# Optimization experiments

Hardware: AMD Instinct MI355X
Metric: run time of the kernel (lower is better)

## Reference

```python
import jax, jax.numpy as jnp
import numpy as np

MAX_ANGLES = 6
SCALES = 2
BN_EPS = 1e-5


def _gauss(k):
    # Gaussian filter init used by WaveletTransform1D (kernel_size k, sigma=k/4)
    xs = np.arange(k, dtype=np.float32) - k // 2
    w = np.exp(-xs ** 2 / (2.0 * (k / 4.0) ** 2)).astype(np.float32)
    return jnp.asarray((w / w.sum()).reshape(1, 1, k))


def setup_inputs():
    key = jax.random.key(0)
    ks = jax.random.split(key, 8)
    B, C, H, W = 8, 64, 128, 128
    return {
        "x": jax.random.normal(ks[0], (B, C, H, W), jnp.float32),
        "lin1_w": jax.random.normal(ks[1], (32, C * 16), jnp.float32) * 0.02,
        "lin1_b": jnp.zeros((32,), jnp.float32),
        "lin2_w": jax.random.normal(ks[2], (MAX_ANGLES, 32), jnp.float32) * 0.02,
        "lin2_b": jnp.zeros((MAX_ANGLES,), jnp.float32),
        "wf0": _gauss(3),
        "wf1": _gauss(5),
        "fuse_w": jax.random.normal(ks[3], (C, C * SCALES), jnp.float32) * 0.05,
        "fuse_b": jax.random.normal(ks[4], (C,), jnp.float32) * 0.05,
        "bn_gamma": jnp.ones((C,), jnp.float32),
        "bn_beta": jnp.zeros((C,), jnp.float32),
        "bn_mean": jnp.zeros((C,), jnp.float32),
        "bn_var": jnp.ones((C,), jnp.float32),
    }


def _grid_sample(img, grid):
    # torch F.grid_sample, bilinear, align_corners=True, padding_mode='zeros'
    N, C, H, W = img.shape
    ix = (grid[..., 0] + 1.0) * 0.5 * (W - 1)  # (N,Hg,Wg)
    iy = (grid[..., 1] + 1.0) * 0.5 * (H - 1)
    x0 = jnp.floor(ix)
    y0 = jnp.floor(iy)
    wx = ix - x0
    wy = iy - y0

    def gather(xi, yi):
        valid = (xi >= 0) & (xi <= W - 1) & (yi >= 0) & (yi <= H - 1)
        xc = jnp.clip(xi, 0, W - 1).astype(jnp.int32)
        yc = jnp.clip(yi, 0, H - 1).astype(jnp.int32)
        v = jax.vmap(lambda im, yy, xx: im[:, yy, xx])(img, yc, xc)  # (N,C,Hg,Wg)
        return v * valid[:, None, :, :].astype(img.dtype)

    v00 = gather(x0, y0)
    v01 = gather(x0 + 1, y0)
    v10 = gather(x0, y0 + 1)
    v11 = gather(x0 + 1, y0 + 1)
    return (v00 * ((1 - wx) * (1 - wy))[:, None]
            + v01 * (wx * (1 - wy))[:, None]
            + v10 * ((1 - wx) * wy)[:, None]
            + v11 * (wx * wy)[:, None])


def _interp1d(x, Lout):
    # F.interpolate mode='linear', align_corners=False, over last axis
    Lin = x.shape[-1]
    real = jnp.clip((jnp.arange(Lout, dtype=jnp.float32) + 0.5) * (Lin / Lout) - 0.5, 0.0, Lin - 1.0)
    i0 = jnp.floor(real).astype(jnp.int32)
    i1 = jnp.minimum(i0 + 1, Lin - 1)
    w = real - i0
    return x[..., i0] * (1.0 - w) + x[..., i1] * w


def _interp_last_ac(x, Lout):
    # linear interp over last axis, align_corners=True
    Lin = x.shape[-1]
    if Lin == Lout:
        return x
    pos = jnp.arange(Lout, dtype=jnp.float32) * ((Lin - 1) / (Lout - 1))
    i0 = jnp.floor(pos).astype(jnp.int32)
    i1 = jnp.minimum(i0 + 1, Lin - 1)
    w = pos - i0
    return x[..., i0] * (1.0 - w) + x[..., i1] * w


def _avgpool1(x):
    L = x.shape[-1]
    return x[..., : (L // 2) * 2].reshape(x.shape[:-1] + (L // 2, 2)).mean(-1)


def _conv1(sig, w):
    # sig (N,1,L), w (1,1,k), 'same' padding cross-correlation (matches torch Conv1d)
    k = w.shape[-1]
    return jax.lax.conv_general_dilated(sig, w, (1,), [(k // 2, k // 2)],
                                        dimension_numbers=("NCH", "OIH", "NCH"))


def reference(x, lin1_w, lin1_b, lin2_w, lin2_b, wf0, wf1, fuse_w, fuse_b,
              bn_gamma, bn_beta, bn_mean, bn_var):
    B, C, H, W = x.shape
    K = MAX_ANGLES
    # --- AnglePredictor: adaptive avg pool 4x4 (H,W divisible by 4) + MLP ---
    pooled = x.reshape(B, C, 4, H // 4, 4, W // 4).mean(axis=(3, 5))  # (B,C,4,4)
    feat = pooled.reshape(B, C * 16)
    h = jax.nn.relu(feat @ lin1_w.T + lin1_b)
    off = (h @ lin2_w.T + lin2_b) * 30.0
    base = jnp.linspace(0.0, 180.0, K)
    angles = jnp.sort(jnp.clip(base[None, :] + off, 0.0, 180.0), axis=1)  # (B,K)
    # --- RadonTransform: per-angle rotation grid + grid_sample + sum over W ---
    xs = jnp.linspace(-1.0, 1.0, W)
    ys = jnp.linspace(-1.0, 1.0, H)
    yc, xc = jnp.meshgrid(ys, xs, indexing="ij")
    th = angles * (jnp.pi / 180.0)
    co = jnp.cos(th)[:, :, None, None]
    si = jnp.sin(th)[:, :, None, None]
    gx = xc[None, None] * co + yc[None, None] * si
    gy = -xc[None, None] * si + yc[None, None] * co
    grid = jnp.stack([gx, gy], axis=-1).reshape(B * K, H, W, 2)
    xexp = jnp.broadcast_to(x[:, None], (B, K, C, H, W)).reshape(B * K, C, H, W)
    rotated = _grid_sample(xexp, grid)          # (B*K,C,H,W)
    sig = rotated.sum(axis=3)                   # (B*K,C,H) == sinogram permuted
    # --- WaveletTransform1D (2 scales, L=H=128 > 4) ---
    N = B * K
    c0 = _conv1(sig.reshape(N * C, 1, H), wf0).reshape(N, C, H)
    cur = _avgpool1(sig)                        # (N,C,H//2)
    L2 = H // 2
    f1 = _conv1(cur.reshape(N * C, 1, L2), wf1)
    u1 = _interp1d(_avgpool1(f1), L2).reshape(N, C, L2)
    c1 = _interp1d(u1, H)                       # resized to target length H
    coeffs = jnp.stack([c0, c1], axis=2)        # (N,C,SCALES,H)
    wav = coeffs.reshape(B, K, C, SCALES, H).transpose(0, 2, 4, 3, 1)  # (B,C,H,S,K)
    combined = wav.reshape(B, C * SCALES, H, K)  # matches torch .view on contiguous
    # --- bilinear align_corners=True resize (H,K)->(H,W), separable ---
    combined = _interp_last_ac(combined, W)
    combined = _interp_last_ac(combined.swapaxes(-1, -2), H).swapaxes(-1, -2)
    # --- fusion: 1x1 conv + BatchNorm(eval) + ReLU ---
    out = jnp.einsum("oc,bchw->bohw", fuse_w, combined) + fuse_b[None, :, None, None]
    scale = (bn_gamma / jnp.sqrt(bn_var + BN_EPS))[None, :, None, None]
    out = (out - bn_mean[None, :, None, None]) * scale + bn_beta[None, :, None, None]
    return jax.nn.relu(out)
```

## Files before the change

### kernel.cpp

```cpp
#include <hip/hip_runtime.h>
#include <hip/hip_fp16.h>
#include <math.h>

#define BB 8
#define CC 64
#define HH 128
#define WW 128
#define KK 6

#define FEAT_OFF 0
#define COEF_OFF 8192

#define WSTR 133
#define NROW 132
#define IMGW (NROW * WSTR)

typedef __fp16   h2  __attribute__((ext_vector_type(2)));
typedef _Float16 hf2 __attribute__((ext_vector_type(2)));

#if __has_builtin(__builtin_amdgcn_fdot2)
#define FDOT2(A, B) __builtin_amdgcn_fdot2(__builtin_bit_cast(hf2, (A)), \
                                           __builtin_bit_cast(hf2, (B)), 0.f, false)
#define FDOT2A(A, B, C) __builtin_amdgcn_fdot2(__builtin_bit_cast(hf2, (A)), \
                                               __builtin_bit_cast(hf2, (B)), (C), false)
#define HAVE_FDOT2 1
#endif

__global__ __launch_bounds__(256) void k_pool(const float* __restrict__ x,
                                              float* __restrict__ ws) {
    int bc = blockIdx.x;
    int b = bc >> 6, c = bc & 63;
    int t = threadIdx.x;
    __shared__ float pool_l[16];
    if (t < 16) pool_l[t] = 0.f;
    __syncthreads();
    const float4* img4 = (const float4*)(x + (size_t)bc * 16384);
    float acc[4] = {0.f, 0.f, 0.f, 0.f};
    int cb = (t & 31) >> 3;
    #pragma unroll
    for (int r = 0; r < 16; ++r) {
        float4 v = img4[r * 256 + t];
        acc[r >> 2] += (v.x + v.y) + (v.z + v.w);
    }
    #pragma unroll
    for (int rb = 0; rb < 4; ++rb)
        atomicAdd(&pool_l[rb * 4 + cb], acc[rb]);
    __syncthreads();
    if (t < 16)
        ws[FEAT_OFF + b * 1024 + c * 16 + t] = pool_l[t] * (1.0f / 1024.0f);
}

#ifdef HAVE_FDOT2
#define SAMPLE(RR, CC, ACC) do {                                   \
    float fr_ = floorf(RR), fc_ = floorf(CC);                      \
    float wr_ = (RR) - fr_, wc_ = (CC) - fc_;                      \
    h2 wv_ = __builtin_amdgcn_cvt_pkrtz(1.0f - wc_, wc_);          \
    int idx_ = (int)fmaf(fr_, 133.f, fc_);                         \
    h2 tp_ = wb2[idx_];                                            \
    h2 bt_ = wb2[idx_ + WSTR];                                     \
    float top_ = FDOT2(wv_, tp_);                                  \
    float d_ = FDOT2A(wv_, bt_, -top_);                            \
    ACC = fmaf(wr_, d_, ACC + top_);                               \
} while (0)
#else
#define SAMPLE(RR, CC, ACC) do {                                   \
    float fr_ = floorf(RR), fc_ = floorf(CC);                      \
    float wr_ = (RR) - fr_, wc_ = (CC) - fc_;                      \
    int idx_ = (int)fmaf(fr_, 133.f, fc_);                         \
    h2 tp_ = wb2[idx_];                                            \
    h2 bt_ = wb2[idx_ + WSTR];                                     \
    float t0_ = fmaf(wc_, (float)tp_.y - (float)tp_.x, (float)tp_.x); \
    float t1_ = fmaf(wc_, (float)bt_.y - (float)bt_.x, (float)bt_.x); \
    ACC += fmaf(wr_, t1_ - t0_, t0_);                              \
} while (0)
#endif

__device__ __forceinline__ void line_bounds(float co, float si, float ix0,
                                            float iy0, int& wA, int& wB) {
    float ic = 1.0f / co, is = 1.0f / (-si);
    float a1 = (-1.0f - ix0) * ic, a2 = (128.0f - ix0) * ic;
    float b1 = (-1.0f - iy0) * is, b2 = (128.0f - iy0) * is;
    float wlo = fmaxf(fminf(a1, a2), fminf(b1, b2));
    float whi = fminf(fmaxf(a1, a2), fmaxf(b1, b2));
    wA = max((int)ceilf(fmaxf(fminf(wlo, 200.f), -200.f)), 0);
    wB = min((int)floorf(fmaxf(fminf(whi, 200.f), -200.f)), 127);
    while (wA <= wB) {
        float cx = fmaf((float)wA, co, ix0), ry = fmaf((float)wA, -si, iy0);
        if (cx >= -1.f && cx <= 128.f && ry >= -1.f && ry <= 128.f) break;
        ++wA;
    }
    while (wB >= wA) {
        float cx = fmaf((float)wB, co, ix0), ry = fmaf((float)wB, -si, iy0);
        if (cx >= -1.f && cx <= 128.f && ry >= -1.f && ry <= 128.f) break;
        --wB;
    }
}

__device__ __forceinline__ float radon_line(const h2* wb2, float co,
                                            float si, float ix0, float iy0,
                                            int wA, int wB) {
    int n = wB - wA + 1;
    float rr0 = fmaf((float)wA, -si, iy0);
    float cc0 = fmaf((float)wA,  co, ix0);
    float rr1 = rr0 - si, cc1 = cc0 + co;
    float rr2 = rr1 - si, cc2 = cc1 + co;
    float rr3 = rr2 - si, cc3 = cc2 + co;
    float rr4 = rr3 - si, cc4 = cc3 + co;
    float rr5 = rr4 - si, cc5 = cc4 + co;
    float rr6 = rr5 - si, cc6 = cc5 + co;
    float rr7 = rr6 - si, cc7 = cc6 + co;
    float si8 = 8.0f * si, co8 = 8.0f * co;
    float a0 = 0.f, a1 = 0.f, a2 = 0.f, a3 = 0.f;
    float a4 = 0.f, a5 = 0.f, a6 = 0.f, a7 = 0.f;
    int i = n;
    while (i >= 8) {
        SAMPLE(rr0, cc0, a0);
        SAMPLE(rr1, cc1, a1);
        SAMPLE(rr2, cc2, a2);
        SAMPLE(rr3, cc3, a3);
        SAMPLE(rr4, cc4, a4);
        SAMPLE(rr5, cc5, a5);
        SAMPLE(rr6, cc6, a6);
        SAMPLE(rr7, cc7, a7);
        rr0 -= si8; cc0 += co8;
        rr1 -= si8; cc1 += co8;
        rr2 -= si8; cc2 += co8;
        rr3 -= si8; cc3 += co8;
        rr4 -= si8; cc4 += co8;
        rr5 -= si8; cc5 += co8;
        rr6 -= si8; cc6 += co8;
        rr7 -= si8; cc7 += co8;
        i -= 8;
    }
    if (i > 0) SAMPLE(rr0, cc0, a0);
    if (i > 1) SAMPLE(rr1, cc1, a1);
    if (i > 2) SAMPLE(rr2, cc2, a2);
    if (i > 3) SAMPLE(rr3, cc3, a3);
    if (i > 4) SAMPLE(rr4, cc4, a4);
    if (i > 5) SAMPLE(rr5, cc5, a5);
    if (i > 6) SAMPLE(rr6, cc6, a6);
    return ((a0 + a1) + (a2 + a3)) + ((a4 + a5) + (a6 + a7));
}

__global__ __launch_bounds__(512, 4) void k_radon(const float* __restrict__ x,
                                                  const float* __restrict__ lin1_w,
                                                  const float* __restrict__ lin1_b,
                                                  const float* __restrict__ lin2_w,
                                                  const float* __restrict__ lin2_b,
                                                  const float* __restrict__ wf0,
                                                  const float* __restrict__ wf1,
                                                  float* __restrict__ ws) {
    int bc = blockIdx.x;
    int b = bc >> 6, c = bc & 63;
    int t = threadIdx.x;
    __shared__ h2 imgh[IMGW];
    __shared__ float sigl[768];
    __shared__ float feat_l[8 * 132];
    __shared__ float h_l[32];
    __shared__ float ang_l[6], ang_s[6];
    __shared__ float co_l[6], si_l[6];

    const h2 z2 = {(__fp16)0.f, (__fp16)0.f};
    for (int i = t; i < 2 * WSTR; i += 512) {
        imgh[i] = z2;
        imgh[130 * WSTR + i] = z2;
    }
    if (t < 128) {
        h2* r = imgh + (t + 2) * WSTR;
        r[0] = z2;
        r[130] = z2;
    }
    const float4* src4 = (const float4*)(x + (size_t)bc * 16384);
    for (int i = t; i < 4096; i += 512) {
        float4 v = src4[i];
        float nxt = __shfl_down(v.x, 1);
        int j = i & 31, row = i >> 5;
        if (j == 31) nxt = 0.f;
        h2* d = imgh + (row + 2) * WSTR + (j << 2) + 2;
        d[0] = __builtin_amdgcn_cvt_pkrtz(v.x, v.y);
        d[1] = __builtin_amdgcn_cvt_pkrtz(v.y, v.z);
        d[2] = __builtin_amdgcn_cvt_pkrtz(v.z, v.w);
        d[3] = __builtin_amdgcn_cvt_pkrtz(v.w, nxt);
        if (j == 0)
            imgh[(row + 2) * WSTR + 1] = __builtin_amdgcn_cvt_pkrtz(0.f, v.x);
    }
    const float* feat = ws + FEAT_OFF + b * 1024;
    for (int i = t; i < 1024; i += 512)
        feat_l[(i >> 7) * 132 + (i & 127)] = feat[i];
    __syncthreads();
    if (t < 256) {
        int m = t >> 3, part = t & 7;
        const float4* wrow = (const float4*)(lin1_w + m * 1024 + part * 128);
        const float4* frow = (const float4*)(feat_l + part * 132);
        float acc = 0.f;
        #pragma unroll 8
        for (int i = 0; i < 32; ++i) {
            float4 wv = wrow[i], fv = frow[i];
            acc = fmaf(wv.x, fv.x, acc); acc = fmaf(wv.y, fv.y, acc);
            acc = fmaf(wv.z, fv.z, acc); acc = fmaf(wv.w, fv.w, acc);
        }
        acc += __shfl_xor(acc, 1);
        acc += __shfl_xor(acc, 2);
        acc += __shfl_xor(acc, 4);
        if (part == 0) h_l[m] = fmaxf(acc + lin1_b[m], 0.f);
    }
    __syncthreads();
    if (t < 6) {
        float a = lin2_b[t];
        #pragma unroll
        for (int i = 0; i < 32; ++i) a = fmaf(h_l[i], lin2_w[t * 32 + i], a);
        a = 36.0f * (float)t + a * 30.0f;
        ang_l[t] = fminf(fmaxf(a, 0.f), 180.f);
    }
    __syncthreads();
    if (t == 0) {
        float v[6];
        #pragma unroll
        for (int i = 0; i < 6; ++i) v[i] = ang_l[i];
        for (int i = 1; i < 6; ++i) {
            float key = v[i]; int j = i - 1;
            while (j >= 0 && v[j] > key) { v[j + 1] = v[j]; --j; }
            v[j + 1] = key;
        }
        #pragma unroll
        for (int i = 0; i < 6; ++i) ang_s[i] = v[i];
    }
    __syncthreads();
    if (t < 6) {
        float th = ang_s[t] * (3.14159265358979323846f / 180.0f);
        co_l[t] = cosf(th);
        si_l[t] = sinf(th);
    }
    __syncthreads();

    const h2* wb2 = imgh + 2 * WSTR + 2;

    {
        int p = t, k = p >> 7, h = p & 127;
        float co = co_l[k], si = si_l[k];
        float yc = fmaf((float)h, 2.0f / 127.0f, -1.0f);
        float ix0 = (fmaf(yc, si, -co) + 1.0f) * 63.5f;
        float iy0 = (fmaf(yc, co,  si) + 1.0f) * 63.5f;
        int wA, wB;
        line_bounds(co, si, ix0, iy0, wA, wB);
        sigl[p] = radon_line(wb2, co, si, ix0, iy0, wA, wB);
    }
    {
        int p = 512 + (t >> 1), k = p >> 7, h = p & 127;
        int half = t & 1;
        float co = co_l[k], si = si_l[k];
        float yc = fmaf((float)h, 2.0f / 127.0f, -1.0f);
        float ix0 = (fmaf(yc, si, -co) + 1.0f) * 63.5f;
        float iy0 = (fmaf(yc, co,  si) + 1.0f) * 63.5f;
        int wA, wB;
        line_bounds(co, si, ix0, iy0, wA, wB);
        int mid = wA + ((wB - wA + 1) >> 1);
        int sA = half ? mid : wA;
        int sB = half ? wB : (mid - 1);
        float a = radon_line(wb2, co, si, ix0, iy0, sA, sB);
        a += __shfl_xor(a, 1);
        if (half == 0) sigl[p] = a;
    }
    __syncthreads();

    float* scr = (float*)imgh;
    float* cur = scr;
    float* f1  = scr + 384;
    float* p1  = scr + 768;
    float* u1  = scr + 960;
    float g0 = wf0[0], g1 = wf0[1], g2 = wf0[2];

    for (int p = t; p < 768; p += 512) {
        int k = p >> 7, h = p & 127;
        const float* s = sigl + k * 128;
        float sm1 = (h > 0)   ? s[h - 1] : 0.f;
        float sp1 = (h < 127) ? s[h + 1] : 0.f;
        float c0 = sm1 * g0 + s[h] * g1 + sp1 * g2;
        ws[COEF_OFF + (((b * 6 + k) * 64 + c) * 2 + 0) * 128 + h] = c0;
    }
    for (int q = t; q < 384; q += 512) {
        int k = q >> 6, l = q & 63;
        cur[q] = (sigl[k * 128 + 2 * l] + sigl[k * 128 + 2 * l + 1]) * 0.5f;
    }
    __syncthreads();

    float w10 = wf1[0], w11 = wf1[1], w12 = wf1[2], w13 = wf1[3], w14 = wf1[4];
    for (int q = t; q < 384; q += 512) {
        int k = q >> 6, l = q & 63;
        const float* cu = cur + k * 64;
        float a = cu[l] * w12;
        a += (l >= 2)  ? cu[l - 2] * w10 : 0.f;
        a += (l >= 1)  ? cu[l - 1] * w11 : 0.f;
        a += (l <= 62) ? cu[l + 1] * w13 : 0.f;
        a += (l <= 61) ? cu[l + 2] * w14 : 0.f;
        f1[q] = a;
    }
    __syncthreads();

    for (int q = t; q < 192; q += 512) {
        int k = q >> 5, m = q & 31;
        p1[q] = (f1[k * 64 + 2 * m] + f1[k * 64 + 2 * m + 1]) * 0.5f;
    }
    __syncthreads();

    for (int q = t; q < 384; q += 512) {
        int k = q >> 6, l = q & 63;
        float real = fminf(fmaxf(0.5f * (float)l - 0.25f, 0.f), 31.f);
        int i0 = (int)real;
        int i1 = min(i0 + 1, 31);
        float wv = real - (float)i0;
        u1[q] = p1[k * 32 + i0] * (1.f - wv) + p1[k * 32 + i1] * wv;
    }
    __syncthreads();

    for (int p = t; p < 768; p += 512) {
        int k = p >> 7, h = p & 127;
        float real = fminf(fmaxf(0.5f * (float)h - 0.25f, 0.f), 63.f);
        int i0 = (int)real;
        int i1 = min(i0 + 1, 63);
        float wv = real - (float)i0;
        float c1 = u1[k * 64 + i0] * (1.f - wv) + u1[k * 64 + i1] * wv;
        ws[COEF_OFF + (((b * 6 + k) * 64 + c) * 2 + 1) * 128 + h] = c1;
    }
}

__global__ __launch_bounds__(256) void k_fuseout(const float* __restrict__ fuse_w,
                                                 const float* __restrict__ fuse_b,
                                                 const float* __restrict__ bn_gamma,
                                                 const float* __restrict__ bn_beta,
                                                 const float* __restrict__ bn_mean,
                                                 const float* __restrict__ bn_var,
                                                 const float* __restrict__ ws,
                                                 float* __restrict__ out) {
    int blk = blockIdx.x;
    int b = blk >> 5, oh = (blk >> 4) & 1, j = blk & 15;
    int t = threadIdx.x;
    __shared__ float M_l[6 * 128 * 8];
    __shared__ float W_l[32 * 129];
    __shared__ float S_l[32 * 8 * 6];

    for (int i = t; i < 6144; i += 256) {
        int x4 = i & 3, half = (i >> 2) & 1, s = (i >> 3) & 1;
        int cc = (i >> 4) & 63, k = i >> 10;
        int hp = half * 64 + 4 * j + x4;
        int c2 = 2 * cc + half;
        int h2p = 2 * x4 + s;
        M_l[(k * 128 + c2) * 8 + h2p] =
            ws[COEF_OFF + (((b * 6 + k) * 64 + cc) * 2 + s) * 128 + hp];
    }
    for (int i = t; i < 4096; i += 256) {
        int op = i >> 7, c2 = i & 127;
        W_l[op * 129 + c2] = fuse_w[(oh * 32 + op) * 128 + c2];
    }
    __syncthreads();

    {
        int op = t >> 3, h2p = t & 7;
        float acc[6] = {0.f, 0.f, 0.f, 0.f, 0.f, 0.f};
        const float* wrow = W_l + op * 129;
        #pragma unroll 4
        for (int c2 = 0; c2 < 128; ++c2) {
            float wv = wrow[c2];
            const float* m = M_l + c2 * 8 + h2p;
            #pragma unroll
            for (int k = 0; k < 6; ++k)
                acc[k] = fmaf(wv, m[k * 1024], acc[k]);
        }
        int o = oh * 32 + op;
        float scale = bn_gamma[o] * rsqrtf(bn_var[o] + 1e-5f);
        float shift = (fuse_b[o] - bn_mean[o]) * scale + bn_beta[o];
        float* srow = S_l + (op * 8 + h2p) * 6;
        #pragma unroll
        for (int k = 0; k < 6; ++k)
            srow[k] = fmaf(acc[k], scale, shift);
    }
    __syncthreads();

    for (int it = 0; it < 128; ++it) {
        int flat = it * 256 + t;
        int w = flat & 127, row = flat >> 7;
        float pos = (float)w * (5.0f / 127.0f);
        int i0 = min((int)pos, 5);
        int i1 = min(i0 + 1, 5);
        float tt = pos - (float)i0;
        const float* srow = S_l + row * 6;
        float val = srow[i0] * (1.f - tt) + srow[i1] * tt;
        int o = oh * 32 + (row >> 3);
        int h2 = 8 * j + (row & 7);
        out[(((b * 64 + o) * 128) + h2) * 128 + w] = fmaxf(val, 0.f);
    }
}

extern "C" void kernel_launch(void* const* d_in, const int* in_sizes, int n_in,
                              void* d_out, int out_size, void* d_ws, size_t ws_size,
                              hipStream_t stream) {
    const float* x        = (const float*)d_in[0];
    const float* lin1_w   = (const float*)d_in[1];
    const float* lin1_b   = (const float*)d_in[2];
    const float* lin2_w   = (const float*)d_in[3];
    const float* lin2_b   = (const float*)d_in[4];
    const float* wf0      = (const float*)d_in[5];
    const float* wf1      = (const float*)d_in[6];
    const float* fuse_w   = (const float*)d_in[7];
    const float* fuse_b   = (const float*)d_in[8];
    const float* bn_gamma = (const float*)d_in[9];
    const float* bn_beta  = (const float*)d_in[10];
    const float* bn_mean  = (const float*)d_in[11];
    const float* bn_var   = (const float*)d_in[12];
    float* ws  = (float*)d_ws;
    float* out = (float*)d_out;

    hipLaunchKernelGGL(k_pool,    dim3(BB * CC), dim3(256), 0, stream, x, ws);
    hipLaunchKernelGGL(k_radon,   dim3(BB * CC), dim3(512), 0, stream,
                       x, lin1_w, lin1_b, lin2_w, lin2_b, wf0, wf1, ws);
    hipLaunchKernelGGL(k_fuseout, dim3(256),     dim3(256), 0, stream,
                       fuse_w, fuse_b, bn_gamma, bn_beta, bn_mean, bn_var,
                       ws, out);
}
```

Measured before the change: 168.7 us.

## Batch radon sample loads before evaluation and split fuseout across more blocks

```diff
diff --git a/kernel.cpp b/kernel.cpp
--- a/kernel.cpp
+++ b/kernel.cpp
@@ -51,16 +51,24 @@
 }
 
 #ifdef HAVE_FDOT2
+#define SAMPLE_LOAD(RR, CC, WV, WR, TP, BT) do {                   \
+    float fr_ = floorf(RR), fc_ = floorf(CC);                      \
+    WR = (RR) - fr_;                                               \
+    float wc_ = (CC) - fc_;                                        \
+    WV = __builtin_amdgcn_cvt_pkrtz(1.0f - wc_, wc_);              \
+    int idx_ = (int)fmaf(fr_, 133.f, fc_);                         \
+    TP = wb2[idx_];                                                \
+    BT = wb2[idx_ + WSTR];                                         \
+} while (0)
+#define SAMPLE_EVAL(WV, WR, TP, BT, ACC) do {                      \
+    float top_ = FDOT2(WV, TP);                                    \
+    float d_ = FDOT2A(WV, BT, -top_);                              \
+    ACC = fmaf(WR, d_, ACC + top_);                                \
+} while (0)
 #define SAMPLE(RR, CC, ACC) do {                                   \
-    float fr_ = floorf(RR), fc_ = floorf(CC);                      \
-    float wr_ = (RR) - fr_, wc_ = (CC) - fc_;                      \
-    h2 wv_ = __builtin_amdgcn_cvt_pkrtz(1.0f - wc_, wc_);          \
-    int idx_ = (int)fmaf(fr_, 133.f, fc_);                         \
-    h2 tp_ = wb2[idx_];                                            \
-    h2 bt_ = wb2[idx_ + WSTR];                                     \
-    float top_ = FDOT2(wv_, tp_);                                  \
-    float d_ = FDOT2A(wv_, bt_, -top_);                            \
-    ACC = fmaf(wr_, d_, ACC + top_);                               \
+    h2 wv_s; float wr_s; h2 tp_s, bt_s;                            \
+    SAMPLE_LOAD(RR, CC, wv_s, wr_s, tp_s, bt_s);                   \
+    SAMPLE_EVAL(wv_s, wr_s, tp_s, bt_s, ACC);                      \
 } while (0)
 #else
 #define SAMPLE(RR, CC, ACC) do {                                   \
@@ -113,15 +121,28 @@
     float a0 = 0.f, a1 = 0.f, a2 = 0.f, a3 = 0.f;
     float a4 = 0.f, a5 = 0.f, a6 = 0.f, a7 = 0.f;
     int i = n;
+#ifdef HAVE_FDOT2
     while (i >= 8) {
-        SAMPLE(rr0, cc0, a0);
-        SAMPLE(rr1, cc1, a1);
-        SAMPLE(rr2, cc2, a2);
-        SAMPLE(rr3, cc3, a3);
-        SAMPLE(rr4, cc4, a4);
-        SAMPLE(rr5, cc5, a5);
-        SAMPLE(rr6, cc6, a6);
-        SAMPLE(rr7, cc7, a7);
+        h2 wv0, wv1, wv2, wv3, wv4, wv5, wv6, wv7;
+        float wr0, wr1, wr2, wr3, wr4, wr5, wr6, wr7;
+        h2 tp0, tp1, tp2, tp3, tp4, tp5, tp6, tp7;
+        h2 bt0, bt1, bt2, bt3, bt4, bt5, bt6, bt7;
+        SAMPLE_LOAD(rr0, cc0, wv0, wr0, tp0, bt0);
+        SAMPLE_LOAD(rr1, cc1, wv1, wr1, tp1, bt1);
+        SAMPLE_LOAD(rr2, cc2, wv2, wr2, tp2, bt2);
+        SAMPLE_LOAD(rr3, cc3, wv3, wr3, tp3, bt3);
+        SAMPLE_LOAD(rr4, cc4, wv4, wr4, tp4, bt4);
+        SAMPLE_LOAD(rr5, cc5, wv5, wr5, tp5, bt5);
+        SAMPLE_LOAD(rr6, cc6, wv6, wr6, tp6, bt6);
+        SAMPLE_LOAD(rr7, cc7, wv7, wr7, tp7, bt7);
+        SAMPLE_EVAL(wv0, wr0, tp0, bt0, a0);
+        SAMPLE_EVAL(wv1, wr1, tp1, bt1, a1);
+        SAMPLE_EVAL(wv2, wr2, tp2, bt2, a2);
+        SAMPLE_EVAL(wv3, wr3, tp3, bt3, a3);
+        SAMPLE_EVAL(wv4, wr4, tp4, bt4, a4);
+        SAMPLE_EVAL(wv5, wr5, tp5, bt5, a5);
+        SAMPLE_EVAL(wv6, wr6, tp6, bt6, a6);
+        SAMPLE_EVAL(wv7, wr7, tp7, bt7, a7);
         rr0 -= si8; cc0 += co8;
         rr1 -= si8; cc1 += co8;
         rr2 -= si8; cc2 += co8;
@@ -132,6 +153,19 @@
         rr7 -= si8; cc7 += co8;
         i -= 8;
     }
+#else
+    while (i >= 8) {
+        SAMPLE(rr0, cc0, a0); SAMPLE(rr1, cc1, a1);
+        SAMPLE(rr2, cc2, a2); SAMPLE(rr3, cc3, a3);
+        SAMPLE(rr4, cc4, a4); SAMPLE(rr5, cc5, a5);
+        SAMPLE(rr6, cc6, a6); SAMPLE(rr7, cc7, a7);
+        rr0 -= si8; cc0 += co8; rr1 -= si8; cc1 += co8;
+        rr2 -= si8; cc2 += co8; rr3 -= si8; cc3 += co8;
+        rr4 -= si8; cc4 += co8; rr5 -= si8; cc5 += co8;
+        rr6 -= si8; cc6 += co8; rr7 -= si8; cc7 += co8;
+        i -= 8;
+    }
+#endif
     if (i > 0) SAMPLE(rr0, cc0, a0);
     if (i > 1) SAMPLE(rr1, cc1, a1);
     if (i > 2) SAMPLE(rr2, cc2, a2);
@@ -324,59 +358,74 @@
     }
 }
 
-__global__ __launch_bounds__(256) void k_fuseout(const float* __restrict__ fuse_w,
-                                                 const float* __restrict__ fuse_b,
-                                                 const float* __restrict__ bn_gamma,
-                                                 const float* __restrict__ bn_beta,
-                                                 const float* __restrict__ bn_mean,
-                                                 const float* __restrict__ bn_var,
-                                                 const float* __restrict__ ws,
-                                                 float* __restrict__ out) {
+__global__ __launch_bounds__(256, 4) void k_fuseout(const float* __restrict__ fuse_w,
+                                                    const float* __restrict__ fuse_b,
+                                                    const float* __restrict__ bn_gamma,
+                                                    const float* __restrict__ bn_beta,
+                                                    const float* __restrict__ bn_mean,
+                                                    const float* __restrict__ bn_var,
+                                                    const float* __restrict__ ws,
+                                                    float* __restrict__ out) {
     int blk = blockIdx.x;
-    int b = blk >> 5, oh = (blk >> 4) & 1, j = blk & 15;
+    int b = blk >> 7, oq = (blk >> 5) & 3, j = blk & 31;
     int t = threadIdx.x;
-    __shared__ float M_l[6 * 128 * 8];
-    __shared__ float W_l[32 * 129];
-    __shared__ float S_l[32 * 8 * 6];
-
-    for (int i = t; i < 6144; i += 256) {
-        int x4 = i & 3, half = (i >> 2) & 1, s = (i >> 3) & 1;
-        int cc = (i >> 4) & 63, k = i >> 10;
-        int hp = half * 64 + 4 * j + x4;
+    __shared__ float M_l[6 * 128 * 4];
+    __shared__ float W_l[16 * 132];
+    __shared__ float P_l[4 * 16 * 4 * 6];
+    __shared__ float S_l[16 * 4 * 6];
+
+    for (int i = t; i < 1536; i += 256) {
+        int half = i & 1, s = (i >> 1) & 1, cc = (i >> 2) & 63, k = i >> 8;
+        const float* src = ws + COEF_OFF +
+            (((b * 6 + k) * 64 + cc) * 2 + s) * 128 + half * 64 + 2 * j;
+        float v0 = src[0], v1 = src[1];
         int c2 = 2 * cc + half;
-        int h2p = 2 * x4 + s;
-        M_l[(k * 128 + c2) * 8 + h2p] =
-            ws[COEF_OFF + (((b * 6 + k) * 64 + cc) * 2 + s) * 128 + hp];
-    }
-    for (int i = t; i < 4096; i += 256) {
+        float* d = M_l + (k * 128 + c2) * 4;
+        d[s] = v0;
+        d[2 + s] = v1;
+    }
+    for (int i = t; i < 2048; i += 256) {
         int op = i >> 7, c2 = i & 127;
-        W_l[op * 129 + c2] = fuse_w[(oh * 32 + op) * 128 + c2];
-    }
-    __syncthreads();
-
+        W_l[op * 132 + c2] = fuse_w[(oq * 16 + op) * 128 + c2];
+    }
+    __syncthreads();
+
+    int cq = t >> 6, op = (t >> 2) & 15, h2p = t & 3;
     {
-        int op = t >> 3, h2p = t & 7;
         float acc[6] = {0.f, 0.f, 0.f, 0.f, 0.f, 0.f};
-        const float* wrow = W_l + op * 129;
+        const float* wrow = W_l + op * 132 + cq * 32;
+        const float* mbase = M_l + (cq * 32) * 4 + h2p;
         #pragma unroll 4
-        for (int c2 = 0; c2 < 128; ++c2) {
+        for (int c2 = 0; c2 < 32; ++c2) {
             float wv = wrow[c2];
-            const float* m = M_l + c2 * 8 + h2p;
+            const float* m = mbase + c2 * 4;
             #pragma unroll
             for (int k = 0; k < 6; ++k)
-                acc[k] = fmaf(wv, m[k * 1024], acc[k]);
+                acc[k] = fmaf(wv, m[k * 512], acc[k]);
         }
-        int o = oh * 32 + op;
+        float* prow = P_l + ((cq * 16 + op) * 4 + h2p) * 6;
+        #pragma unroll
+        for (int k = 0; k < 6; ++k)
+            prow[k] = acc[k];
+    }
+    __syncthreads();
+
+    if (cq == 0) {
+        int o = oq * 16 + op;
         float scale = bn_gamma[o] * rsqrtf(bn_var[o] + 1e-5f);
         float shift = (fuse_b[o] - bn_mean[o]) * scale + bn_beta[o];
-        float* srow = S_l + (op * 8 + h2p) * 6;
+        int base = (op * 4 + h2p) * 6;
+        float* srow = S_l + base;
         #pragma unroll
-        for (int k = 0; k < 6; ++k)
-            srow[k] = fmaf(acc[k], scale, shift);
-    }
-    __syncthreads();
-
-    for (int it = 0; it < 128; ++it) {
+        for (int k = 0; k < 6; ++k) {
+            float v = P_l[base + k] + P_l[384 + base + k]
+                    + P_l[768 + base + k] + P_l[1152 + base + k];
+            srow[k] = fmaf(v, scale, shift);
+        }
+    }
+    __syncthreads();
+
+    for (int it = 0; it < 32; ++it) {
         int flat = it * 256 + t;
         int w = flat & 127, row = flat >> 7;
         float pos = (float)w * (5.0f / 127.0f);
@@ -385,8 +434,8 @@
         float tt = pos - (float)i0;
         const float* srow = S_l + row * 6;
         float val = srow[i0] * (1.f - tt) + srow[i1] * tt;
-        int o = oh * 32 + (row >> 3);
-        int h2 = 8 * j + (row & 7);
+        int o = oq * 16 + (row >> 2);
+        int h2 = 4 * j + (row & 3);
         out[(((b * 64 + o) * 128) + h2) * 128 + w] = fmaxf(val, 0.f);
     }
 }
@@ -413,7 +462,7 @@
     hipLaunchKernelGGL(k_pool,    dim3(BB * CC), dim3(256), 0, stream, x, ws);
     hipLaunchKernelGGL(k_radon,   dim3(BB * CC), dim3(512), 0, stream,
                        x, lin1_w, lin1_b, lin2_w, lin2_b, wf0, wf1, ws);
-    hipLaunchKernelGGL(k_fuseout, dim3(256),     dim3(256), 0, stream,
+    hipLaunchKernelGGL(k_fuseout, dim3(1024),    dim3(256), 0, stream,
                        fuse_w, fuse_b, bn_gamma, bn_beta, bn_mean, bn_var,
                        ws, out);
 }
```

After: 163.6 us. -3.0%, faster.
